# Performance work log

Hardware: AMD Instinct MI355X
Metric: run time of the kernel (lower is better)

The kernel has to match this reference:

```python
import jax, jax.numpy as jnp
import numpy as np
import math

MAX_SIZE = 2048  # max_size init arg


def setup_inputs() -> dict:
    key = jax.random.key(0)
    k1, k2, k3 = jax.random.split(key, 3)
    B, S, D = 16, 1024, 512
    PRED = 256
    data = jax.random.normal(k1, (B, S, D), dtype=jnp.float32)
    W = jax.random.normal(k2, (PRED, D), dtype=jnp.float32) * (1.0 / math.sqrt(D))
    b = jax.random.normal(k3, (PRED,), dtype=jnp.float32) * 0.01
    return {"data": data, "W": W, "b": b}


def reference(data, W, b):
    # data: [B, S, D]; self-attention with q=k=v=data
    B, S, D = data.shape
    pred_len = W.shape[0]
    scale = 1.0 / math.sqrt(D)
    scores = jnp.einsum('bsd,btd->bst', data, data) * scale          # [B,S,S]
    prob = jax.nn.softmax(scores, axis=-1)
    attn = jnp.einsum('bst,btd->bsd', prob, data)                     # [B,S,D]
    # NOTE: the original concatenates a 'mask' block (rows S..2S) onto attn,
    # but the per-timestep Linear loop only reads rows 0..S-1, so the mask
    # never affects the output (dead code). The loop collapses to one GEMM.
    lin = jnp.einsum('bsd,pd->bsp', attn, W) + b                      # [B,S,pred_len]
    out = jnp.zeros((B, MAX_SIZE, pred_len), dtype=data.dtype)
    out = out.at[:, :S, :].set(lin)
    return out
```

## Files before the change

### kernel.cpp

```cpp
#include <hip/hip_runtime.h>
#include <cstdint>
#include <cstddef>

#define B_    16
#define S_    1024
#define D_    512
#define P_    256
#define MAXS_ 2048

typedef unsigned short u16;
typedef unsigned int   u32;
typedef _Float16 f16;
typedef _Float16 f16x8 __attribute__((ext_vector_type(8)));
typedef float  f32x4  __attribute__((ext_vector_type(4)));
typedef unsigned short u16x4 __attribute__((ext_vector_type(4)));
typedef unsigned short u16x8 __attribute__((ext_vector_type(8)));

__device__ __forceinline__ void gld_lds16(const void* g, void* l) {
  __builtin_amdgcn_global_load_lds(
      (const __attribute__((address_space(1))) u32*)g,
      (__attribute__((address_space(3))) u32*)l, 16, 0, 0);
}

__device__ __forceinline__ u16 f2h(float f) {
  return __builtin_bit_cast(u16, (f16)f);
}
__device__ __forceinline__ float h2f(u16 h) {
  return (float)__builtin_bit_cast(f16, h);
}

__global__ void convert_f16_kernel(const float* __restrict__ src, u16* __restrict__ dst, long n4) {
  long stride = (long)gridDim.x * blockDim.x;
  for (long i = (long)blockIdx.x * blockDim.x + threadIdx.x; i < n4; i += stride) {
    float4 v = ((const float4*)src)[i];
    u16x4 o;
    o[0] = f2h(v.x); o[1] = f2h(v.y); o[2] = f2h(v.z); o[3] = f2h(v.w);
    ((u16x4*)dst)[i] = o;
  }
}

__global__ __launch_bounds__(512, 2) void qk_pipe(
    const u16* __restrict__ A, u16* __restrict__ Cout, float scale) {
  extern __shared__ __align__(16) char smem[];
  const int tid  = threadIdx.x;
  const int lane = tid & 63;
  const int w    = tid >> 6;
  const int wm   = w >> 2;
  const int wn   = w & 3;
  const int lr   = lane & 15;
  const int hi   = lane >> 4;

  const int bz = blockIdx.z;
  const int I0 = blockIdx.y * 256;
  const int J0 = blockIdx.x * 256;
  const u16* Ab = A + (long)bz * (S_ * D_);

  auto stageP = [&](int s, int part) {
    if (s >= 16) return;
    char* dst = smem + (s & 3) * 32768 + part * 16384;
    const int base = part ? J0 : I0;
    const int k0 = s * 32;
    #pragma unroll
    for (int i = 0; i < 2; ++i) {
      int cid   = i * 512 + tid;
      int inner = cid >> 2;
      int c     = (cid & 3) ^ ((inner >> 1) & 3);
      gld_lds16(Ab + (size_t)(base + inner) * D_ + k0 + c * 8, dst + cid * 16);
    }
  };

  f32x4 acc[8][4] = {};

  stageP(0, 0); stageP(0, 1);
  stageP(1, 0); stageP(1, 1);
  stageP(2, 0); stageP(2, 1);
  asm volatile("s_waitcnt vmcnt(8)" ::: "memory");
  __builtin_amdgcn_s_barrier();

  for (int s = 0; s < 16; ++s) {
    const char* sl = smem + (s & 3) * 32768;
    f16x8 bf[4];
    {
      f16x8 af[4];
      #pragma unroll
      for (int mq = 0; mq < 4; ++mq) {
        int row = wm * 128 + mq * 16 + lr;
        int cp  = hi ^ ((row >> 1) & 3);
        af[mq] = *(const f16x8*)(sl + row * 64 + cp * 16);
      }
      #pragma unroll
      for (int n = 0; n < 4; ++n) {
        int row = wn * 64 + n * 16 + lr;
        int cp  = hi ^ ((row >> 1) & 3);
        bf[n] = *(const f16x8*)(sl + 16384 + row * 64 + cp * 16);
      }
      stageP(s + 3, 0);
      __builtin_amdgcn_s_barrier();
      asm volatile("s_waitcnt lgkmcnt(0)" ::: "memory");
      __builtin_amdgcn_sched_barrier(0);
      __builtin_amdgcn_s_setprio(1);
      #pragma unroll
      for (int mq = 0; mq < 4; ++mq)
        #pragma unroll
        for (int n = 0; n < 4; ++n)
          acc[mq][n] = __builtin_amdgcn_mfma_f32_16x16x32_f16(af[mq], bf[n], acc[mq][n], 0, 0, 0);
      __builtin_amdgcn_s_setprio(0);
      __builtin_amdgcn_s_barrier();
    }
    {
      f16x8 af[4];
      #pragma unroll
      for (int mq = 0; mq < 4; ++mq) {
        int row = wm * 128 + 64 + mq * 16 + lr;
        int cp  = hi ^ ((row >> 1) & 3);
        af[mq] = *(const f16x8*)(sl + row * 64 + cp * 16);
      }
      stageP(s + 3, 1);
      __builtin_amdgcn_s_barrier();
      asm volatile("s_waitcnt lgkmcnt(0)" ::: "memory");
      __builtin_amdgcn_sched_barrier(0);
      __builtin_amdgcn_s_setprio(1);
      #pragma unroll
      for (int mq = 0; mq < 4; ++mq)
        #pragma unroll
        for (int n = 0; n < 4; ++n)
          acc[4 + mq][n] = __builtin_amdgcn_mfma_f32_16x16x32_f16(af[mq], bf[n], acc[4 + mq][n], 0, 0, 0);
      __builtin_amdgcn_s_setprio(0);
      if (s <= 12)      asm volatile("s_waitcnt vmcnt(8)" ::: "memory");
      else if (s == 13) asm volatile("s_waitcnt vmcnt(4)" ::: "memory");
      else if (s == 14) asm volatile("s_waitcnt vmcnt(0)" ::: "memory");
      __builtin_amdgcn_s_barrier();
    }
  }

  u16* Cb = Cout + (long)bz * S_ * S_;
  const int row0 = I0 + wm * 128;
  const int col0 = J0 + wn * 64;
  #pragma unroll
  for (int m = 0; m < 8; ++m) {
    #pragma unroll
    for (int i = 0; i < 4; ++i) {
      int r = row0 + m * 16 + (hi << 2) + i;
      #pragma unroll
      for (int n = 0; n < 4; ++n) {
        int c = col0 + n * 16 + lr;
        Cb[(size_t)r * S_ + c] = f2h(acc[m][n][i] * scale);
      }
    }
  }
}

__global__ __launch_bounds__(256) void stats_kernel(
    const u16* __restrict__ scores, float2* __restrict__ rowstat) {
  const int lane = threadIdx.x & 63;
  const int wv   = threadIdx.x >> 6;
  const long row = (long)blockIdx.x * 4 + wv;
  const u16* src = scores + row * S_;

  u16x8 a0 = *(const u16x8*)&src[lane * 16];
  u16x8 a1 = *(const u16x8*)&src[lane * 16 + 8];
  float v[16];
  #pragma unroll
  for (int j = 0; j < 8; ++j) { v[j] = h2f(a0[j]); v[8 + j] = h2f(a1[j]); }

  float mx = v[0];
  #pragma unroll
  for (int j = 1; j < 16; ++j) mx = fmaxf(mx, v[j]);
  #pragma unroll
  for (int off = 32; off > 0; off >>= 1)
    mx = fmaxf(mx, __shfl_xor(mx, off));

  const float l2e = 1.4426950408889634f;
  float sum = 0.f;
  #pragma unroll
  for (int j = 0; j < 16; ++j) sum += exp2f((v[j] - mx) * l2e);
  #pragma unroll
  for (int off = 32; off > 0; off >>= 1)
    sum += __shfl_xor(sum, off);

  if (lane == 0) rowstat[row] = make_float2(mx, 1.f / sum);
}

__global__ __launch_bounds__(256, 2) void pv_kernel(
    const u16* __restrict__ scores, const u16* __restrict__ VWT,
    const float2* __restrict__ rowstat,
    float* __restrict__ out, const float* __restrict__ bias) {
  extern __shared__ __align__(16) char smem[];
  const int tid  = threadIdx.x;
  const int lane = tid & 63;
  const int wn   = tid >> 6;
  const int bz = blockIdx.z;
  const int yt = blockIdx.y;

  float* ob = out + (long)bz * MAXS_ * P_;
  if (yt >= 32) {
    float4* o = (float4*)(ob + (size_t)yt * 32 * P_);
    for (int i = tid; i < 32 * P_ / 4; i += 256)
      o[i] = make_float4(0.f, 0.f, 0.f, 0.f);
    return;
  }

  const int q0 = yt * 32;
  const u16* sb = scores + ((long)bz * S_ + q0) * S_;
  const u16* Vb = VWT + (long)bz * P_ * S_;

  const int arow = tid >> 3;
  const int ac   = tid & 7;
  float2 st = rowstat[(long)bz * S_ + q0 + arow];
  const float am = st.x, ail = st.y;
  const float l2e = 1.4426950408889634f;

  auto stageB = [&](int t) {
    char* dB = smem + 8192 + (t & 1) * 32768;
    const int k0 = t * 64;
    #pragma unroll
    for (int i = 0; i < 8; ++i) {
      int cid = i * 256 + tid;
      int row = cid >> 3;
      int c   = (cid & 7) ^ (row & 7);
      gld_lds16(Vb + (size_t)row * S_ + k0 + c * 8, dB + cid * 16);
    }
  };
  auto writeA = [&](int buf, u16x8 r0) {
    u16x8 p0;
    #pragma unroll
    for (int j = 0; j < 8; ++j)
      p0[j] = f2h(exp2f((h2f(r0[j]) - am) * l2e) * ail);
    int c = ac ^ (arow & 7);
    *(u16x8*)(smem + buf * 4096 + (arow * 8 + c) * 16) = p0;
  };

  f32x4 acc[2][4] = {};
  u16x8 anx;

  anx = *(const u16x8*)(sb + (size_t)arow * S_ + ac * 8);
  __builtin_amdgcn_sched_barrier(0);
  stageB(0);
  __builtin_amdgcn_sched_barrier(0);
  asm volatile("s_waitcnt vmcnt(8)" ::: "memory");
  writeA(0, anx);
  asm volatile("s_waitcnt vmcnt(0) lgkmcnt(0)" ::: "memory");
  __builtin_amdgcn_s_barrier();

  for (int t = 0; t < 16; ++t) {
    const char* lA = smem + (t & 1) * 4096;
    const char* lB = smem + 8192 + (t & 1) * 32768;

    if (t < 15) {
      anx = *(const u16x8*)(sb + (size_t)arow * S_ + (t + 1) * 64 + ac * 8);
      __builtin_amdgcn_sched_barrier(0);
      stageB(t + 1);
      __builtin_amdgcn_sched_barrier(0);
    }

    #pragma unroll
    for (int kk = 0; kk < 2; ++kk) {
      f16x8 af[2], bf[4];
      #pragma unroll
      for (int m = 0; m < 2; ++m) {
        int row = m * 16 + (lane & 15);
        int cp  = (kk * 4 + (lane >> 4)) ^ (row & 7);
        af[m] = *(const f16x8*)(lA + ((row * 8 + cp) << 4));
      }
      #pragma unroll
      for (int n = 0; n < 4; ++n) {
        int row = wn * 64 + n * 16 + (lane & 15);
        int cp  = (kk * 4 + (lane >> 4)) ^ (row & 7);
        bf[n] = *(const f16x8*)(lB + ((row * 8 + cp) << 4));
      }
      __builtin_amdgcn_s_setprio(1);
      #pragma unroll
      for (int m = 0; m < 2; ++m)
        #pragma unroll
        for (int n = 0; n < 4; ++n)
          acc[m][n] = __builtin_amdgcn_mfma_f32_16x16x32_f16(af[m], bf[n], acc[m][n], 0, 0, 0);
      __builtin_amdgcn_s_setprio(0);
    }

    if (t < 15) {
      asm volatile("s_waitcnt vmcnt(8)" ::: "memory");
      writeA((t + 1) & 1, anx);
      asm volatile("s_waitcnt vmcnt(0) lgkmcnt(0)" ::: "memory");
      __builtin_amdgcn_s_barrier();
    }
  }

  const int lr = lane & 15, hi = lane >> 4;
  const int col0 = wn * 64;
  float bv[4];
  #pragma unroll
  for (int n = 0; n < 4; ++n) bv[n] = bias[col0 + n * 16 + lr];
  #pragma unroll
  for (int m = 0; m < 2; ++m) {
    #pragma unroll
    for (int i = 0; i < 4; ++i) {
      int r = q0 + m * 16 + (hi << 2) + i;
      #pragma unroll
      for (int n = 0; n < 4; ++n)
        ob[(size_t)r * P_ + col0 + n * 16 + lr] = acc[m][n][i] + bv[n];
    }
  }
}

template<int KK, int BM, int BN, int NW, int WNS>
__global__ __launch_bounds__(NW * 64, 2) void gemm_nt_small(
    const u16* __restrict__ A, const u16* __restrict__ Bm,
    u16* __restrict__ C, long sAb, long sBb, long sCb, int LDC) {
  constexpr int T   = NW * 64;
  constexpr int WMS = NW / WNS;
  constexpr int MF  = BM / (WMS * 16);
  constexpr int NF  = BN / (WNS * 16);
  constexpr int LA  = BM * 8 / T;
  constexpr int LB  = BN * 8 / T;
  constexpr int SZ  = (BM + BN) * 128;
  constexpr int NT  = KK / 64;

  extern __shared__ __align__(16) char smem[];
  const int tid  = threadIdx.x;
  const int lane = tid & 63;
  const int w    = tid >> 6;
  const int wm   = w / WNS;
  const int wn   = w % WNS;
  const int lr   = lane & 15;
  const int hi   = lane >> 4;

  const int bz = blockIdx.z;
  const int I0 = blockIdx.y * BM;
  const int J0 = blockIdx.x * BN;
  const u16* Ab = A  + (long)bz * sAb;
  const u16* Bb = Bm + (long)bz * sBb;

  auto stage = [&](int buf, int k0) {
    char* sA = smem + buf * SZ;
    char* sB = sA + BM * 128;
    #pragma unroll
    for (int i = 0; i < LA; ++i) {
      int cid = i * T + tid;
      int row = cid >> 3;
      int c   = (cid & 7) ^ (row & 7);
      gld_lds16(Ab + (size_t)(I0 + row) * KK + k0 + c * 8, sA + cid * 16);
    }
    #pragma unroll
    for (int i = 0; i < LB; ++i) {
      int cid = i * T + tid;
      int row = cid >> 3;
      int c   = (cid & 7) ^ (row & 7);
      gld_lds16(Bb + (size_t)(J0 + row) * KK + k0 + c * 8, sB + cid * 16);
    }
  };

  f32x4 acc[MF][NF] = {};
  stage(0, 0);
  for (int t = 0; t < NT; ++t) {
    const char* lA = smem + (t & 1) * SZ;
    const char* lB = lA + BM * 128;
    if (t + 1 < NT) {
      stage((t + 1) & 1, (t + 1) * 64);
      asm volatile("s_waitcnt vmcnt(%0)" :: "i"(LA + LB) : "memory");
    } else {
      asm volatile("s_waitcnt vmcnt(0)" ::: "memory");
    }
    __builtin_amdgcn_s_barrier();
    __builtin_amdgcn_sched_barrier(0);
    #pragma unroll
    for (int kk = 0; kk < 2; ++kk) {
      f16x8 af[MF], bfv[NF];
      #pragma unroll
      for (int m = 0; m < MF; ++m) {
        int row = wm * (MF * 16) + m * 16 + lr;
        int cp  = (kk * 4 + hi) ^ (row & 7);
        af[m] = *(const f16x8*)(lA + ((row * 8 + cp) << 4));
      }
      #pragma unroll
      for (int n = 0; n < NF; ++n) {
        int row = wn * (NF * 16) + n * 16 + lr;
        int cp  = (kk * 4 + hi) ^ (row & 7);
        bfv[n] = *(const f16x8*)(lB + ((row * 8 + cp) << 4));
      }
      __builtin_amdgcn_s_setprio(1);
      #pragma unroll
      for (int m = 0; m < MF; ++m)
        #pragma unroll
        for (int n = 0; n < NF; ++n)
          acc[m][n] = __builtin_amdgcn_mfma_f32_16x16x32_f16(af[m], bfv[n], acc[m][n], 0, 0, 0);
      __builtin_amdgcn_s_setprio(0);
    }
    __builtin_amdgcn_sched_barrier(0);
    __builtin_amdgcn_s_barrier();
  }

  const int row0 = I0 + wm * (MF * 16);
  const int col0 = J0 + wn * (NF * 16);
  #pragma unroll
  for (int m = 0; m < MF; ++m)
    #pragma unroll
    for (int i = 0; i < 4; ++i) {
      int r = row0 + m * 16 + (hi << 2) + i;
      #pragma unroll
      for (int n = 0; n < NF; ++n)
        C[(long)bz * sCb + (size_t)r * LDC + col0 + n * 16 + lr] = f2h(acc[m][n][i]);
    }
}

extern "C" void kernel_launch(void* const* d_in, const int* in_sizes, int n_in,
                              void* d_out, int out_size, void* d_ws, size_t ws_size,
                              hipStream_t stream) {
  const float* data = (const float*)d_in[0];
  const float* W    = (const float*)d_in[1];
  const float* bias = (const float*)d_in[2];
  float* out = (float*)d_out;
  char*  ws  = (char*)d_ws;

  const size_t MB = 1024 * 1024;
  u16*    dataH   = (u16*)(ws);
  u16*    Wh      = (u16*)(ws + 16 * MB);
  u16*    scoresH = (u16*)(ws + 17 * MB);
  u16*    VWT     = (u16*)(ws + 49 * MB);
  float2* rowstat = (float2*)(ws + 57 * MB);

  const float scale = 0.04419417382415922f;

  constexpr int SMEM_QK = 4 * 32768;
  constexpr int SMEM_PV = 2 * 4096 + 2 * 32768;
  constexpr int SMEM_VW = 2 * (64 + 128) * 128;

  (void)hipFuncSetAttribute((const void*)&qk_pipe,
                      hipFuncAttributeMaxDynamicSharedMemorySize, SMEM_QK);
  (void)hipFuncSetAttribute((const void*)&pv_kernel,
                      hipFuncAttributeMaxDynamicSharedMemorySize, SMEM_PV);
  (void)hipFuncSetAttribute((const void*)&gemm_nt_small<512, 64, 128, 4, 2>,
                      hipFuncAttributeMaxDynamicSharedMemorySize, SMEM_VW);

  convert_f16_kernel<<<2048, 256, 0, stream>>>(data, dataH, (long)B_ * S_ * D_ / 4);
  convert_f16_kernel<<<64, 256, 0, stream>>>(W, Wh, (long)P_ * D_ / 4);

  gemm_nt_small<512, 64, 128, 4, 2><<<dim3(8, 4, 16), 256, SMEM_VW, stream>>>(
      Wh, dataH, VWT, 0L, (long)S_ * D_, (long)P_ * S_, S_);

  qk_pipe<<<dim3(4, 4, 16), 512, SMEM_QK, stream>>>(dataH, scoresH, scale);

  stats_kernel<<<4096, 256, 0, stream>>>(scoresH, rowstat);

  pv_kernel<<<dim3(1, 64, 16), 256, SMEM_PV, stream>>>(
      scoresH, VWT, rowstat, out, bias);
}
```

Before: 83.23 us.

## Rewrite PV kernel to stream operands from global into registers without LDS

Replaces the LDS-staged, double-buffered PV GEMM with a kernel that loads MFMA fragments directly from global memory into registers, using ping-pong register buffers. It retiles to a 4x16 grid where each block covers 128 query rows by 64 output columns, and each wave owns 32 rows. The softmax normalisation moves from every probability element to a single multiply per output row in the epilogue. This removes LDS traffic and barriers, but scores are now reread once per column block (4x) and the direct global loads are uncoalesced 16-byte chunks.

```diff
diff --git a/kernel.cpp b/kernel.cpp
--- a/kernel.cpp
+++ b/kernel.cpp
@@ -181,123 +181,89 @@
   if (lane == 0) rowstat[row] = make_float2(mx, 1.f / sum);
 }
 
-__global__ __launch_bounds__(256, 2) void pv_kernel(
+__global__ __launch_bounds__(256, 2) void pv_stream(
     const u16* __restrict__ scores, const u16* __restrict__ VWT,
     const float2* __restrict__ rowstat,
     float* __restrict__ out, const float* __restrict__ bias) {
-  extern __shared__ __align__(16) char smem[];
   const int tid  = threadIdx.x;
   const int lane = tid & 63;
-  const int wn   = tid >> 6;
-  const int bz = blockIdx.z;
-  const int yt = blockIdx.y;
+  const int wm   = tid >> 6;
+  const int lr   = lane & 15;
+  const int hi   = lane >> 4;
+  const int bz   = blockIdx.z;
+  const int yt   = blockIdx.y;
 
   float* ob = out + (long)bz * MAXS_ * P_;
-  if (yt >= 32) {
-    float4* o = (float4*)(ob + (size_t)yt * 32 * P_);
-    for (int i = tid; i < 32 * P_ / 4; i += 256)
+  if (yt >= 8) {
+    float4* o = (float4*)(ob + (size_t)yt * 128 * P_);
+    for (int i = tid; i < 128 * P_ / 4; i += 256)
       o[i] = make_float4(0.f, 0.f, 0.f, 0.f);
     return;
   }
 
-  const int q0 = yt * 32;
-  const u16* sb = scores + ((long)bz * S_ + q0) * S_;
-  const u16* Vb = VWT + (long)bz * P_ * S_;
-
-  const int arow = tid >> 3;
-  const int ac   = tid & 7;
-  float2 st = rowstat[(long)bz * S_ + q0 + arow];
-  const float am = st.x, ail = st.y;
+  const int q0 = yt * 128;
+  const int J0 = blockIdx.x * 64;
+  const int r0 = q0 + wm * 32;
+  const u16* sA = scores + ((long)bz * S_ + r0) * S_;
+  const u16* sB = VWT + (long)bz * P_ * S_ + (size_t)J0 * S_;
   const float l2e = 1.4426950408889634f;
 
-  auto stageB = [&](int t) {
-    char* dB = smem + 8192 + (t & 1) * 32768;
-    const int k0 = t * 64;
-    #pragma unroll
-    for (int i = 0; i < 8; ++i) {
-      int cid = i * 256 + tid;
-      int row = cid >> 3;
-      int c   = (cid & 7) ^ (row & 7);
-      gld_lds16(Vb + (size_t)row * S_ + k0 + c * 8, dB + cid * 16);
-    }
+  const float nml0 = -rowstat[(long)bz * S_ + r0 + lr].x * l2e;
+  const float nml1 = -rowstat[(long)bz * S_ + r0 + 16 + lr].x * l2e;
+
+  f32x4 acc[2][4] = {};
+
+  u16x8 a0[2], b0[4], a1[2], b1[4];
+
+  auto loadAll = [&](u16x8 (&a)[2], u16x8 (&b)[4], int t) {
+    const int k = t * 32 + hi * 8;
+    #pragma unroll
+    for (int m = 0; m < 2; ++m)
+      a[m] = *(const u16x8*)(sA + (size_t)(m * 16 + lr) * S_ + k);
+    #pragma unroll
+    for (int n = 0; n < 4; ++n)
+      b[n] = *(const u16x8*)(sB + (size_t)(n * 16 + lr) * S_ + k);
   };
-  auto writeA = [&](int buf, u16x8 r0) {
-    u16x8 p0;
-    #pragma unroll
-    for (int j = 0; j < 8; ++j)
-      p0[j] = f2h(exp2f((h2f(r0[j]) - am) * l2e) * ail);
-    int c = ac ^ (arow & 7);
-    *(u16x8*)(smem + buf * 4096 + (arow * 8 + c) * 16) = p0;
+  auto compute = [&](u16x8 (&a)[2], u16x8 (&b)[4]) {
+    f16x8 pa[2];
+    #pragma unroll
+    for (int m = 0; m < 2; ++m) {
+      const float nml = m ? nml1 : nml0;
+      #pragma unroll
+      for (int j = 0; j < 8; ++j)
+        pa[m][j] = (f16)exp2f(fmaf(h2f(a[m][j]), l2e, nml));
+    }
+    #pragma unroll
+    for (int m = 0; m < 2; ++m)
+      #pragma unroll
+      for (int n = 0; n < 4; ++n)
+        acc[m][n] = __builtin_amdgcn_mfma_f32_16x16x32_f16(
+            pa[m], __builtin_bit_cast(f16x8, b[n]), acc[m][n], 0, 0, 0);
   };
 
-  f32x4 acc[2][4] = {};
-  u16x8 anx;
-
-  anx = *(const u16x8*)(sb + (size_t)arow * S_ + ac * 8);
-  __builtin_amdgcn_sched_barrier(0);
-  stageB(0);
-  __builtin_amdgcn_sched_barrier(0);
-  asm volatile("s_waitcnt vmcnt(8)" ::: "memory");
-  writeA(0, anx);
-  asm volatile("s_waitcnt vmcnt(0) lgkmcnt(0)" ::: "memory");
-  __builtin_amdgcn_s_barrier();
-
-  for (int t = 0; t < 16; ++t) {
-    const char* lA = smem + (t & 1) * 4096;
-    const char* lB = smem + 8192 + (t & 1) * 32768;
-
-    if (t < 15) {
-      anx = *(const u16x8*)(sb + (size_t)arow * S_ + (t + 1) * 64 + ac * 8);
-      __builtin_amdgcn_sched_barrier(0);
-      stageB(t + 1);
-      __builtin_amdgcn_sched_barrier(0);
-    }
-
-    #pragma unroll
-    for (int kk = 0; kk < 2; ++kk) {
-      f16x8 af[2], bf[4];
-      #pragma unroll
-      for (int m = 0; m < 2; ++m) {
-        int row = m * 16 + (lane & 15);
-        int cp  = (kk * 4 + (lane >> 4)) ^ (row & 7);
-        af[m] = *(const f16x8*)(lA + ((row * 8 + cp) << 4));
-      }
-      #pragma unroll
-      for (int n = 0; n < 4; ++n) {
-        int row = wn * 64 + n * 16 + (lane & 15);
-        int cp  = (kk * 4 + (lane >> 4)) ^ (row & 7);
-        bf[n] = *(const f16x8*)(lB + ((row * 8 + cp) << 4));
-      }
-      __builtin_amdgcn_s_setprio(1);
-      #pragma unroll
-      for (int m = 0; m < 2; ++m)
-        #pragma unroll
-        for (int n = 0; n < 4; ++n)
-          acc[m][n] = __builtin_amdgcn_mfma_f32_16x16x32_f16(af[m], bf[n], acc[m][n], 0, 0, 0);
-      __builtin_amdgcn_s_setprio(0);
-    }
-
-    if (t < 15) {
-      asm volatile("s_waitcnt vmcnt(8)" ::: "memory");
-      writeA((t + 1) & 1, anx);
-      asm volatile("s_waitcnt vmcnt(0) lgkmcnt(0)" ::: "memory");
-      __builtin_amdgcn_s_barrier();
-    }
-  }
-
-  const int lr = lane & 15, hi = lane >> 4;
-  const int col0 = wn * 64;
+  loadAll(a0, b0, 0);
+  for (int t = 0; t < 30; t += 2) {
+    loadAll(a1, b1, t + 1);
+    compute(a0, b0);
+    loadAll(a0, b0, t + 2);
+    compute(a1, b1);
+  }
+  loadAll(a1, b1, 31);
+  compute(a0, b0);
+  compute(a1, b1);
+
   float bv[4];
   #pragma unroll
-  for (int n = 0; n < 4; ++n) bv[n] = bias[col0 + n * 16 + lr];
+  for (int n = 0; n < 4; ++n) bv[n] = bias[J0 + n * 16 + lr];
   #pragma unroll
   for (int m = 0; m < 2; ++m) {
     #pragma unroll
     for (int i = 0; i < 4; ++i) {
-      int r = q0 + m * 16 + (hi << 2) + i;
+      const int r = r0 + m * 16 + (hi << 2) + i;
+      const float il = rowstat[(long)bz * S_ + r].y;
       #pragma unroll
       for (int n = 0; n < 4; ++n)
-        ob[(size_t)r * P_ + col0 + n * 16 + lr] = acc[m][n][i] + bv[n];
+        ob[(size_t)r * P_ + J0 + n * 16 + lr] = acc[m][n][i] * il + bv[n];
     }
   }
 }
@@ -421,13 +387,10 @@
   const float scale = 0.04419417382415922f;
 
   constexpr int SMEM_QK = 4 * 32768;
-  constexpr int SMEM_PV = 2 * 4096 + 2 * 32768;
   constexpr int SMEM_VW = 2 * (64 + 128) * 128;
 
   (void)hipFuncSetAttribute((const void*)&qk_pipe,
                       hipFuncAttributeMaxDynamicSharedMemorySize, SMEM_QK);
-  (void)hipFuncSetAttribute((const void*)&pv_kernel,
-                      hipFuncAttributeMaxDynamicSharedMemorySize, SMEM_PV);
   (void)hipFuncSetAttribute((const void*)&gemm_nt_small<512, 64, 128, 4, 2>,
                       hipFuncAttributeMaxDynamicSharedMemorySize, SMEM_VW);
 
@@ -441,6 +404,6 @@
 
   stats_kernel<<<4096, 256, 0, stream>>>(scoresH, rowstat);
 
-  pv_kernel<<<dim3(1, 64, 16), 256, SMEM_PV, stream>>>(
+  pv_stream<<<dim3(4, 16, 16), 256, 0, stream>>>(
       scoresH, VWT, rowstat, out, bias);
 }
```

New measurement: 145.5 us. 74.9% more time.
